# Kernel optimization log

Hardware: AMD Instinct MI355X
Metric: run time of the kernel (lower is better)

## Reference

```python
import math
import jax, jax.numpy as jnp
import numpy as np

SCORE_THR = 0.05
NMS_THR = 0.5
MIN_SIZE = 0.01
MAX_DET = 100
SCALE_CLAMP = math.log(1000.0 / 16.0)
WX, WY, WW, WH = 10.0, 10.0, 5.0, 5.0  # BoxCoder weights


def setup_inputs() -> dict:
    key = jax.random.key(0)
    k1, k2, k3, k4 = jax.random.split(key, 4)
    B, N, C = 4, 2048, 3
    H = W = 800
    class_logits = 2.0 * jax.random.normal(k1, (B, N, C), dtype=jnp.float32)
    box_regression = 0.5 * jax.random.normal(k2, (B, N, 4 * C), dtype=jnp.float32)
    cxy = jax.random.uniform(k3, (B, N, 2), minval=0.0, maxval=float(W))
    wh = jax.random.uniform(k4, (B, N, 2), minval=4.0, maxval=100.0)
    proposals = jnp.concatenate([cxy - 0.5 * wh, cxy + 0.5 * wh], axis=-1)
    proposals = jnp.clip(proposals, 0.0, float(W))
    return {"class_logits": class_logits, "box_regression": box_regression,
            "proposals": proposals, "image_h": H, "image_w": W}


def _decode(rel, props):
    # rel: [N, C, 4] deltas, props: [N, 4] xyxy -> [N, C, 4] decoded boxes
    w = props[:, 2] - props[:, 0]
    h = props[:, 3] - props[:, 1]
    cx = props[:, 0] + 0.5 * w
    cy = props[:, 1] + 0.5 * h
    dx = rel[..., 0] / WX
    dy = rel[..., 1] / WY
    dw = jnp.minimum(rel[..., 2] / WW, SCALE_CLAMP)
    dh = jnp.minimum(rel[..., 3] / WH, SCALE_CLAMP)
    pcx = dx * w[:, None] + cx[:, None]
    pcy = dy * h[:, None] + cy[:, None]
    pw = jnp.exp(dw) * w[:, None]
    ph = jnp.exp(dh) * h[:, None]
    return jnp.stack([pcx - 0.5 * pw, pcy - 0.5 * ph,
                      pcx + 0.5 * pw, pcy + 0.5 * ph], axis=-1)


def _pairwise_iou(b):
    # b: [M, 4] -> [M, M]
    area = (b[:, 2] - b[:, 0]) * (b[:, 3] - b[:, 1])
    lt = jnp.maximum(b[:, None, :2], b[None, :, :2])
    rb = jnp.minimum(b[:, None, 2:], b[None, :, 2:])
    whd = jnp.clip(rb - lt, 0.0)
    inter = whd[..., 0] * whd[..., 1]
    return inter / (area[:, None] + area[None, :] - inter + 1e-7)


def _per_image(logits, rel, props, H, W):
    N, C = logits.shape
    scores = jax.nn.softmax(logits, axis=-1)               # [N, C]
    boxes = _decode(rel.reshape(N, C, 4), props)           # [N, C, 4]
    # clip to image (x in [0,W], y in [0,H])
    boxes = jnp.stack([jnp.clip(boxes[..., 0], 0.0, W),
                       jnp.clip(boxes[..., 1], 0.0, H),
                       jnp.clip(boxes[..., 2], 0.0, W),
                       jnp.clip(boxes[..., 3], 0.0, H)], axis=-1)
    # drop background class and flatten -> M = N*(C-1)
    boxes = boxes[:, 1:, :].reshape(-1, 4)
    scores = scores[:, 1:].reshape(-1)
    labels = jnp.broadcast_to(jnp.arange(1, C), (N, C - 1)).reshape(-1)
    valid = ((scores > SCORE_THR)
             & (boxes[:, 2] - boxes[:, 0] >= MIN_SIZE)
             & (boxes[:, 3] - boxes[:, 1] >= MIN_SIZE))
    # batched_nms via per-class coordinate offset
    offset = labels.astype(boxes.dtype) * (jnp.max(boxes) + 1.0)
    ob = boxes + offset[:, None]
    sort_key = jnp.where(valid, scores, -jnp.inf)
    order = jnp.argsort(-sort_key)
    bs, ss, ls, vs, obs = boxes[order], scores[order], labels[order], valid[order], ob[order]
    iou = _pairwise_iou(obs)                               # [M, M]
    M = bs.shape[0]
    idxs = jnp.arange(M)
    def body(i, keep):
        sup = keep[i] & (iou[i] > NMS_THR) & (idxs > i)
        return keep & ~sup
    keep = jax.lax.fori_loop(0, M, body, vs)
    sel = jnp.argsort(~keep, stable=True)[:MAX_DET]        # kept first, score order preserved
    kb, ksc, kl, kk = bs[sel], ss[sel], ls[sel], keep[sel]
    kb = jnp.where(kk[:, None], kb, 0.0)
    ksc = jnp.where(kk, ksc, 0.0)
    kl = jnp.where(kk, kl, 0)
    return kb, ksc, kl, kk


def reference(class_logits, box_regression, proposals, image_h, image_w):
    H = jnp.float32(image_h)
    W = jnp.float32(image_w)
    f = jax.vmap(lambda l, r, p: _per_image(l, r, p, H, W))
    boxes, scores, labels, keep = f(class_logits, box_regression, proposals)
    return boxes, scores, labels, keep
```

## Files before the change

### kernel.cpp

```cpp
#include <hip/hip_runtime.h>
#include <stdint.h>

#define BB 4
#define NN 2048
#define CC 3
#define MM (NN * (CC - 1))
#define MAXDET 100
#define SCORE_THR 0.05f
#define NMS_THR 0.5f
#define MIN_SIZE 0.01f
#define TTARGET 256
#define SSKCAP 1024
#define TILE 128

#define SCORE_OFF (BB * MAXDET * 4)
#define LABEL_OFF (SCORE_OFF + BB * MAXDET)
#define KEEP_OFF (LABEL_OFF + BB * MAXDET)
#define STASH(b, j) (SCORE_OFF + (b) * MAXDET + 96 + (j))

__device__ __forceinline__ void wave_lds_sync() {
  __builtin_amdgcn_wave_barrier();
  __builtin_amdgcn_s_waitcnt(0xC07F);
  __builtin_amdgcn_wave_barrier();
}

__device__ __forceinline__ bool iou_gt(const float4 A, const float aA,
                                       const float4 B, const float aB) {
#pragma clang fp contract(off)
  float ltx = fmaxf(A.x, B.x), lty = fmaxf(A.y, B.y);
  float rbx = fminf(A.z, B.z), rby = fminf(A.w, B.w);
  float iw = fmaxf(rbx - ltx, 0.0f), ih = fmaxf(rby - lty, 0.0f);
  float inter = iw * ih;
  float denom = ((aA + aB) - inter) + 1e-7f;
  return inter / denom > NMS_THR;
}

__global__ __launch_bounds__(512) void decode_kernel(const float* __restrict__ logits,
                                                     const float* __restrict__ rel,
                                                     const float* __restrict__ props,
                                                     const int* __restrict__ ph,
                                                     const int* __restrict__ pw,
                                                     float4* __restrict__ cand_box,
                                                     unsigned long long* __restrict__ keys,
                                                     unsigned* __restrict__ hist_g,
                                                     float* __restrict__ out) {
#pragma clang fp contract(off)
  __shared__ float red[512];
  int tid = threadIdx.x;
  int t = blockIdx.x * 512 + tid;
  int b = t >> 11;
  int n = t & 2047;
  float Hf = (float)ph[0];
  float Wf = (float)pw[0];

  const float* lg = logits + (size_t)t * CC;
  float l0 = lg[0], l1 = lg[1], l2 = lg[2];
  float mx = fmaxf(l0, fmaxf(l1, l2));
  float e0 = expf(l0 - mx), e1 = expf(l1 - mx), e2 = expf(l2 - mx);
  float ssum = (e0 + e1) + e2;

  float4 pr = ((const float4*)props)[t];
  float w = pr.z - pr.x, h = pr.w - pr.y;
  float cx = pr.x + 0.5f * w, cy = pr.y + 0.5f * h;
  const float4* rl = (const float4*)(rel + (size_t)t * 12);
  const float SCALE_CLAMP = 4.135166556742356f;

  float lmax = 0.0f;
  for (int c = 1; c < CC; ++c) {
    float4 rv = rl[c];
    float score = (c == 1 ? e1 : e2) / ssum;
    float dx = rv.x / 10.0f;
    float dy = rv.y / 10.0f;
    float dw = fminf(rv.z / 5.0f, SCALE_CLAMP);
    float dh = fminf(rv.w / 5.0f, SCALE_CLAMP);
    float pcx = dx * w + cx;
    float pcy = dy * h + cy;
    float bw = expf(dw) * w;
    float bh = expf(dh) * h;
    float x1 = pcx - 0.5f * bw, y1 = pcy - 0.5f * bh;
    float x2 = pcx + 0.5f * bw, y2 = pcy + 0.5f * bh;
    x1 = fminf(fmaxf(x1, 0.0f), Wf);
    y1 = fminf(fmaxf(y1, 0.0f), Hf);
    x2 = fminf(fmaxf(x2, 0.0f), Wf);
    y2 = fminf(fmaxf(y2, 0.0f), Hf);

    lmax = fmaxf(lmax, fmaxf(fmaxf(x1, y1), fmaxf(x2, y2)));

    bool valid = (score > SCORE_THR) && (x2 - x1 >= MIN_SIZE) && (y2 - y1 >= MIN_SIZE);
    int m = n * (CC - 1) + (c - 1);
    cand_box[(size_t)b * MM + m] = make_float4(x1, y1, x2, y2);
    unsigned long long key = 0ull;
    if (valid) {
      unsigned sb = __float_as_uint(score);
      key = (((unsigned long long)sb) << 32) |
            (unsigned long long)(0xFFFFFFFFu - (unsigned)m);
      atomicAdd(&hist_g[b * 1024 + ((sb >> 16) & 1023)], 1u);
    }
    keys[(size_t)b * MM + m] = key;
  }

  red[tid] = lmax;
  __syncthreads();
  for (int s2 = 256; s2 > 0; s2 >>= 1) {
    if (tid < s2) red[tid] = fmaxf(red[tid], red[tid + s2]);
    __syncthreads();
  }
  if (tid == 0) out[STASH(b, blockIdx.x & 3)] = red[0];
}

__device__ void bitonic_sort_desc(unsigned long long* a, int P, int tid) {
  int prev_big = 1;
  for (int size = 2; size <= P; size <<= 1) {
    for (int stride = size >> 1; stride > 0; stride >>= 1) {
      int big = (stride >= 128);
      if (big | prev_big) __syncthreads(); else wave_lds_sync();
      for (int i = tid; i < (P >> 1); i += 512) {
        int lo = 2 * i - (i & (stride - 1));
        int hi = lo + stride;
        bool asc = ((lo & size) != 0);
        unsigned long long x = a[lo], y = a[hi];
        if ((x > y) == asc) { a[lo] = y; a[hi] = x; }
      }
      prev_big = big;
    }
  }
  __syncthreads();
}

__device__ void bitonic_sort_desc_reg512(unsigned long long* a,
                                         unsigned long long* xbuf0,
                                         unsigned long long* xbuf1,
                                         int T, int tid) {
  unsigned long long v = (tid < T) ? a[tid] : 0ull;
  int xb = 0;
  for (int size = 2; size <= 512; size <<= 1) {
    for (int stride = size >> 1; stride > 0; stride >>= 1) {
      unsigned long long o;
      if (stride < 64) {
        o = __shfl_xor(v, stride);
      } else {
        unsigned long long* buf = xb ? xbuf1 : xbuf0;
        __syncthreads();
        buf[tid] = v;
        __syncthreads();
        o = buf[tid ^ stride];
        xb ^= 1;
      }
      bool is_lo = (tid & stride) == 0;
      bool asc = (tid & size) != 0;
      bool take_min = (asc == is_lo);
      bool o_less = (o < v);
      unsigned long long mn = o_less ? o : v;
      unsigned long long mx = o_less ? v : o;
      v = take_min ? mn : mx;
    }
  }
  __syncthreads();
  a[tid] = v;
  __syncthreads();
}

__device__ int tiled_nms(const unsigned long long* keys_s, int count,
                         const float4* __restrict__ cbg, float off_base,
                         const float4* sboxall, const unsigned short* map, int use_map,
                         float4* tob, float4* trb, float* tarea,
                         ulonglong2* smask, int* sflag, int* knew,
                         float4* kept_ob, float4* kept_raw, float* kept_area,
                         unsigned long long* kept_key, int* s_nnew, int tid) {
#pragma clang fp contract(off)
  int wv = tid >> 6, lane = tid & 63;
  int cnt = 0;
  for (int base = 0; base < count && cnt < MAXDET; base += TILE) {
    int tsz = (count - base < TILE) ? (count - base) : TILE;
    if (tid < tsz) {
      unsigned long long key = keys_s[base + tid];
      int m = (int)(0xFFFFFFFFu - (unsigned)key);
      float4 bx = use_map ? sboxall[map[m]] : cbg[m];
      int lbl = (m & 1) + 1;
      float off = (float)lbl * off_base;
      float4 ob = make_float4(bx.x + off, bx.y + off, bx.z + off, bx.w + off);
      tob[tid] = ob;
      trb[tid] = bx;
      tarea[tid] = (ob.z - ob.x) * (ob.w - ob.y);
    }
    __syncthreads();

    float4 bi0 = tob[lane];
    float ai0 = tarea[lane];
    float4 bi1 = tob[lane + 64];
    float ai1 = tarea[lane + 64];
    float4 kb0 = kept_ob[(lane < cnt) ? lane : 0];
    float ka0 = kept_area[(lane < cnt) ? lane : 0];
    float4 kb1 = kept_ob[(lane + 64 < cnt) ? lane + 64 : 0];
    float ka1 = kept_area[(lane + 64 < cnt) ? lane + 64 : 0];

    for (int j = wv; j < tsz; j += 8) {
      float4 aj = tob[j];
      float aaj = tarea[j];
      unsigned long long w0 = 0ull, w1 = 0ull;
      if (j < 63) {
        bool p = (lane > j) && (lane < tsz) && iou_gt(aj, aaj, bi0, ai0);
        w0 = __ballot(p);
      }
      if (j < 127) {
        int i = lane + 64;
        bool p = (i > j) && (i < tsz) && iou_gt(aj, aaj, bi1, ai1);
        w1 = __ballot(p);
      }
      bool s = false;
      if (cnt > 0) {
        if (lane < cnt && iou_gt(kb0, ka0, aj, aaj)) s = true;
        if (cnt > 64 && lane + 64 < cnt && iou_gt(kb1, ka1, aj, aaj)) s = true;
      }
      int anyk = __any(s);
      if (lane == 0) {
        smask[j].x = w0;
        smask[j].y = w1;
        sflag[j] = anyk;
      }
    }
    __syncthreads();

    if (tid < 64) {
      int iA = 2 * lane, iB = 2 * lane + 1;
      ulonglong2 rA = smask[(iA < tsz) ? iA : 0];
      ulonglong2 rB = smask[(iB < tsz) ? iB : 0];
      int fA = sflag[(iA < tsz) ? iA : 0];
      int fB = sflag[(iB < tsz) ? iB : 0];
      unsigned long long r0 = 0ull, r1 = 0ull;
      int c = cnt, nk = 0;
      for (int j = 0; j < tsz; ++j) {
        int src = j >> 1;
        unsigned long long m0 = __shfl((j & 1) ? rB.x : rA.x, src);
        unsigned long long m1 = __shfl((j & 1) ? rB.y : rA.y, src);
        int fl = __shfl((j & 1) ? fB : fA, src);
        bool rem = (j < 64) ? ((r0 >> j) & 1ull) : ((r1 >> (j - 64)) & 1ull);
        if (!rem && !fl) {
          if (lane == 0) knew[nk] = j;
          nk++;
          c++;
          r0 |= m0;
          r1 |= m1;
          if (c >= MAXDET) break;
        }
      }
      if (lane == 0) *s_nnew = nk;
    }
    __syncthreads();

    int nnew = *s_nnew;
    if (tid < nnew) {
      int j = knew[tid];
      kept_ob[cnt + tid] = tob[j];
      kept_raw[cnt + tid] = trb[j];
      kept_area[cnt + tid] = tarea[j];
      kept_key[cnt + tid] = keys_s[base + j];
    }
    cnt += nnew;
    __syncthreads();
  }
  return cnt;
}

__global__ __launch_bounds__(512) void nms_kernel(const float4* __restrict__ cand_box,
                                                  const unsigned long long* __restrict__ keys,
                                                  const unsigned* __restrict__ hist_g,
                                                  float* __restrict__ out) {
#pragma clang fp contract(off)
  __shared__ __align__(16) unsigned long long sk[MM];
  __shared__ __align__(16) unsigned long long ssk[SSKCAP];
  __shared__ __align__(16) float4 sbox[SSKCAP];
  __shared__ unsigned short map[MM];
  __shared__ __align__(16) float4 tob[TILE];
  __shared__ __align__(16) float4 trb[TILE];
  __shared__ float tarea[TILE];
  __shared__ __align__(16) ulonglong2 smask[TILE];
  __shared__ int sflag[TILE];
  __shared__ int knew[TILE];
  __shared__ float4 kept_ob[MAXDET];
  __shared__ float4 kept_raw[MAXDET];
  __shared__ float kept_area[MAXDET];
  __shared__ unsigned long long kept_key[MAXDET];
  __shared__ int s_scnt, s_thr, s_vtot, s_cnt, s_fb, s_nnew;

  int b = blockIdx.x;
  int tid = threadIdx.x;
  int lane = tid & 63;
  const float4* cbg = cand_box + (size_t)b * MM;

  const ulonglong2* kg = (const ulonglong2*)(keys + (size_t)b * MM);
  ulonglong2 kr[4];
#pragma unroll
  for (int j = 0; j < 4; ++j) kr[j] = kg[j * 512 + tid];

  if (tid == 0) { s_scnt = 0; s_fb = 0; s_cnt = 0; }
  float m01 = fmaxf(out[STASH(b, 0)], out[STASH(b, 1)]);
  float m23 = fmaxf(out[STASH(b, 2)], out[STASH(b, 3)]);
  float off_base = fmaxf(m01, m23) + 1.0f;

  if (tid < 64) {
    const unsigned* hg = hist_g + b * 1024 + tid * 16;
    unsigned own[16];
#pragma unroll
    for (int i = 0; i < 16; ++i) own[i] = hg[i];
    unsigned psum = 0;
#pragma unroll
    for (int i = 0; i < 16; ++i) psum += own[i];
    unsigned s = psum;
    for (int d = 1; d < 64; d <<= 1) {
      unsigned o = __shfl_down(s, d);
      if (tid + d < 64) s += o;
    }
    unsigned after = s - psum;
    int best = -1;
    unsigned run = after;
#pragma unroll
    for (int i = 15; i >= 0; --i) {
      run += own[i];
      if (best < 0 && run >= TTARGET) best = tid * 16 + i;
    }
    int gb = best;
    for (int d = 1; d < 64; d <<= 1) {
      int o = __shfl_down(gb, d);
      if (tid + d < 64) gb = (o > gb) ? o : gb;
    }
    if (tid == 0) {
      s_thr = (gb < 0) ? 0 : gb;
      s_vtot = (int)s;
    }
  }
  __syncthreads();
  int thr = s_thr;
  int Vtot = s_vtot;

#pragma unroll
  for (int j = 0; j < 4; ++j) {
    int m0 = 1024 * j + 2 * tid;
    float4 b0 = cbg[m0];
    float4 b1 = cbg[m0 + 1];
#pragma unroll
    for (int half = 0; half < 2; ++half) {
      unsigned long long key = half ? kr[j].y : kr[j].x;
      unsigned hik = (unsigned)(key >> 32);
      bool pred = (hik != 0u) && ((int)((hik >> 16) & 1023) >= thr);
      unsigned long long mask = __ballot(pred);
      int ofs = __popcll(mask & ((1ull << lane) - 1ull));
      int basea = 0;
      if (lane == 0 && mask) basea = atomicAdd(&s_scnt, (int)__popcll(mask));
      basea = __shfl(basea, 0);
      if (pred) {
        int pos = basea + ofs;
        if (pos < SSKCAP) {
          ssk[pos] = key;
          sbox[pos] = half ? b1 : b0;
          map[m0 + half] = (unsigned short)pos;
        }
      }
    }
  }
  __syncthreads();
  int T = s_scnt;

  if (T <= SSKCAP) {
    if (T <= 512) {
      bitonic_sort_desc_reg512(ssk, sk, sk + 512, T, tid);
    } else {
      int P = 1;
      while (P < T) P <<= 1;
      for (int i = T + tid; i < P; i += 512) ssk[i] = 0ull;
      __syncthreads();
      bitonic_sort_desc(ssk, P, tid);
    }
    int cnt = tiled_nms(ssk, T, cbg, off_base, sbox, map, 1, tob, trb, tarea,
                        smask, sflag, knew, kept_ob, kept_raw, kept_area,
                        kept_key, &s_nnew, tid);
    if (tid == 0) {
      s_cnt = cnt;
      s_fb = (cnt < MAXDET && T < Vtot) ? 1 : 0;
    }
  } else {
    if (tid == 0) s_fb = 1;
  }
  __syncthreads();

  if (s_fb) {
    ulonglong2* skp = (ulonglong2*)sk;
#pragma unroll
    for (int j = 0; j < 4; ++j) skp[j * 512 + tid] = kr[j];
    __syncthreads();
    bitonic_sort_desc(sk, MM, tid);
    int cnt = tiled_nms(sk, Vtot, cbg, off_base, sbox, map, 0, tob, trb, tarea,
                        smask, sflag, knew, kept_ob, kept_raw, kept_area,
                        kept_key, &s_nnew, tid);
    if (tid == 0) s_cnt = cnt;
    __syncthreads();
  }

  int cnt = s_cnt;
  if (tid < MAXDET) {
    float4 bx = make_float4(0.0f, 0.0f, 0.0f, 0.0f);
    float sc = 0.0f, lb = 0.0f, kp = 0.0f;
    if (tid < cnt) {
      unsigned long long key = kept_key[tid];
      int m = (int)(0xFFFFFFFFu - (unsigned)key);
      bx = kept_raw[tid];
      sc = __uint_as_float((unsigned)(key >> 32));
      lb = (float)((m & 1) + 1);
      kp = 1.0f;
    }
    float* obp = out + (size_t)b * MAXDET * 4 + (size_t)tid * 4;
    obp[0] = bx.x; obp[1] = bx.y; obp[2] = bx.z; obp[3] = bx.w;
    out[SCORE_OFF + b * MAXDET + tid] = sc;
    out[LABEL_OFF + b * MAXDET + tid] = lb;
    out[KEEP_OFF + b * MAXDET + tid] = kp;
  }
}

extern "C" void kernel_launch(void* const* d_in, const int* in_sizes, int n_in,
                              void* d_out, int out_size, void* d_ws, size_t ws_size,
                              hipStream_t stream) {
  const float* logits = (const float*)d_in[0];
  const float* rel = (const float*)d_in[1];
  const float* props = (const float*)d_in[2];
  const int* ph = (const int*)d_in[3];
  const int* pw = (const int*)d_in[4];
  float* out = (float*)d_out;

  char* ws = (char*)d_ws;
  float4* cand_box = (float4*)ws;
  unsigned long long* keys = (unsigned long long*)(ws + (size_t)BB * MM * 16);
  unsigned* hist_g = (unsigned*)(ws + (size_t)BB * MM * 16 + (size_t)BB * MM * 8);

  hipMemsetAsync(hist_g, 0, BB * 1024 * sizeof(unsigned), stream);
  decode_kernel<<<16, 512, 0, stream>>>(logits, rel, props, ph, pw, cand_box,
                                        keys, hist_g, out);
  nms_kernel<<<BB, 512, 0, stream>>>(cand_box, keys, hist_g, out);
}
```

Measured before the change: 96.11 us.

## Use per-block LDS histograms, drop memset, and vectorize greedy NMS resolve

The decode kernel now builds its score histogram in shared memory and each block writes its own 1024-bin slice to global memory. The NMS kernel sums the four slices belonging to its image, which removes the global atomics and the separate memset launch. The greedy tile-resolve loop also changes: instead of shuffling rows across lanes it holds the removed/flagged bits as ballot masks and prefetches mask rows from LDS four ahead. This trades global atomic traffic and one launch for extra LDS initialisation and four reads per bin.

```diff
diff --git a/kernel.cpp b/kernel.cpp
--- a/kernel.cpp
+++ b/kernel.cpp
@@ -46,12 +46,17 @@
                                                      float* __restrict__ out) {
 #pragma clang fp contract(off)
   __shared__ float red[512];
+  __shared__ unsigned lhist[1024];
   int tid = threadIdx.x;
   int t = blockIdx.x * 512 + tid;
   int b = t >> 11;
   int n = t & 2047;
   float Hf = (float)ph[0];
   float Wf = (float)pw[0];
+
+  lhist[tid] = 0u;
+  lhist[tid + 512] = 0u;
+  __syncthreads();
 
   const float* lg = logits + (size_t)t * CC;
   float l0 = lg[0], l1 = lg[1], l2 = lg[2];
@@ -94,7 +99,7 @@
       unsigned sb = __float_as_uint(score);
       key = (((unsigned long long)sb) << 32) |
             (unsigned long long)(0xFFFFFFFFu - (unsigned)m);
-      atomicAdd(&hist_g[b * 1024 + ((sb >> 16) & 1023)], 1u);
+      atomicAdd(&lhist[(sb >> 16) & 1023], 1u);
     }
     keys[(size_t)b * MM + m] = key;
   }
@@ -106,6 +111,9 @@
     __syncthreads();
   }
   if (tid == 0) out[STASH(b, blockIdx.x & 3)] = red[0];
+
+  hist_g[blockIdx.x * 1024 + tid] = lhist[tid];
+  hist_g[blockIdx.x * 1024 + tid + 512] = lhist[tid + 512];
 }
 
 __device__ void bitonic_sort_desc(unsigned long long* a, int P, int tid) {
@@ -222,25 +230,26 @@
     __syncthreads();
 
     if (tid < 64) {
-      int iA = 2 * lane, iB = 2 * lane + 1;
-      ulonglong2 rA = smask[(iA < tsz) ? iA : 0];
-      ulonglong2 rB = smask[(iB < tsz) ? iB : 0];
-      int fA = sflag[(iA < tsz) ? iA : 0];
-      int fB = sflag[(iB < tsz) ? iB : 0];
-      unsigned long long r0 = 0ull, r1 = 0ull;
+      bool f0 = (lane < tsz) && (sflag[lane] != 0);
+      unsigned long long remv0 = __ballot(f0);
+      bool f1 = (lane + 64 < tsz) && (sflag[lane + 64] != 0);
+      unsigned long long remv1 = __ballot(f1);
+      ulonglong2 pre[4];
+#pragma unroll
+      for (int k = 0; k < 4; ++k) pre[k] = smask[(k < tsz) ? k : 0];
       int c = cnt, nk = 0;
       for (int j = 0; j < tsz; ++j) {
-        int src = j >> 1;
-        unsigned long long m0 = __shfl((j & 1) ? rB.x : rA.x, src);
-        unsigned long long m1 = __shfl((j & 1) ? rB.y : rA.y, src);
-        int fl = __shfl((j & 1) ? fB : fA, src);
-        bool rem = (j < 64) ? ((r0 >> j) & 1ull) : ((r1 >> (j - 64)) & 1ull);
-        if (!rem && !fl) {
+        ulonglong2 row = pre[j & 3];
+        int nxt = j + 4;
+        pre[j & 3] = smask[(nxt < tsz) ? nxt : 0];
+        bool rem = (j < 64) ? (((remv0 >> j) & 1ull) != 0ull)
+                            : (((remv1 >> (j - 64)) & 1ull) != 0ull);
+        if (!rem) {
           if (lane == 0) knew[nk] = j;
           nk++;
           c++;
-          r0 |= m0;
-          r1 |= m1;
+          remv0 |= row.x;
+          remv1 |= row.y;
           if (c >= MAXDET) break;
         }
       }
@@ -299,10 +308,11 @@
   float off_base = fmaxf(m01, m23) + 1.0f;
 
   if (tid < 64) {
-    const unsigned* hg = hist_g + b * 1024 + tid * 16;
+    const unsigned* hg = hist_g + (b * 4) * 1024 + tid * 16;
     unsigned own[16];
 #pragma unroll
-    for (int i = 0; i < 16; ++i) own[i] = hg[i];
+    for (int i = 0; i < 16; ++i)
+      own[i] = hg[i] + hg[1024 + i] + hg[2048 + i] + hg[3072 + i];
     unsigned psum = 0;
 #pragma unroll
     for (int i = 0; i < 16; ++i) psum += own[i];
@@ -431,7 +441,6 @@
   unsigned long long* keys = (unsigned long long*)(ws + (size_t)BB * MM * 16);
   unsigned* hist_g = (unsigned*)(ws + (size_t)BB * MM * 16 + (size_t)BB * MM * 8);
 
-  hipMemsetAsync(hist_g, 0, BB * 1024 * sizeof(unsigned), stream);
   decode_kernel<<<16, 512, 0, stream>>>(logits, rel, props, ph, pw, cand_box,
                                         keys, hist_g, out);
   nms_kernel<<<BB, 512, 0, stream>>>(cand_box, keys, hist_g, out);
```

New measurement: 94.72 us. Within noise of the previous version (-1.5%).
